# Performance work log

Hardware: AMD Instinct MI355X
Metric: run time of the kernel (lower is better)

Reference implementation:

```python
import jax, jax.numpy as jnp
import numpy as np

H, HD, TOPK = 16, 64, 64

def setup_inputs() -> dict:
    key = jax.random.key(0)
    ks = jax.random.split(key, 6)
    L, B, E = 2048, 2, 1024
    s = 0.02
    return {
        "query": jax.random.normal(ks[0], (L, B, E), jnp.float32),
        "q_w": jax.random.normal(ks[1], (E, E), jnp.float32) * s,
        "q_b": jnp.zeros((E,), jnp.float32),
        "k_w": jax.random.normal(ks[2], (E, E), jnp.float32) * s,
        "k_b": jnp.zeros((E,), jnp.float32),
        "v_w": jax.random.normal(ks[3], (E, E), jnp.float32) * s,
        "v_b": jnp.zeros((E,), jnp.float32),
        "o_w": jax.random.normal(ks[4], (E, E), jnp.float32) * s,
        "o_b": jnp.zeros((E,), jnp.float32),
    }

def reference(query, q_w, q_b, k_w, k_b, v_w, v_b, o_w, o_b):
    L, B, E = query.shape
    scale = HD ** -0.5
    identity = query
    x = jnp.transpose(query, (1, 0, 2))              # [B, L, E]

    def proj(w, b):
        y = x @ w.T + b                              # nn.Linear: x W^T + b
        return jnp.transpose(y.reshape(B, L, H, HD), (0, 2, 1, 3))  # [B,H,L,HD]

    q = proj(q_w, q_b)
    k = proj(k_w, k_b)
    v = proj(v_w, v_b)

    sim_nm = jnp.einsum('bhqd,bhkd->bhqk', q, k) * scale   # full scores [B,H,L,L]
    score_m = sim_nm.sum(axis=2)                           # [B,H,L] per-key score
    _, top_idx = jax.lax.top_k(score_m, TOPK)              # [B,H,TOPK]
    selected_k = jnp.take_along_axis(k, top_idx[..., None], axis=2)  # [B,H,TOPK,HD]

    sim_qn = jax.nn.softmax(jnp.einsum('bhqd,bhmd->bhqm', q, selected_k) * scale, axis=-1)
    sim_km = jax.nn.softmax(jnp.einsum('bhkd,bhmd->bhkm', k, selected_k) * scale, axis=-1)
    sim_qk = jnp.einsum('bhqm,bhkm->bhqk', sim_qn, sim_km)  # [B,H,L,L]
    out = jnp.einsum('bhqk,bhkd->bhqd', sim_qk, v)          # [B,H,L,HD]

    out = jnp.transpose(out, (0, 2, 1, 3)).reshape(B, L, E)
    out = out @ o_w.T + o_b
    out = jnp.transpose(out, (1, 0, 2))                     # back to [L, B, E]
    return identity + out
```

## Files before the change

### kernel.cpp

```cpp
#include <hip/hip_runtime.h>
#include <hip/hip_bf16.h>

#define L_ 2048
#define B_ 2
#define E_ 1024
#define H_ 16
#define HD_ 64
#define TOPK_ 64
#define MROWS (B_*L_)
#define SCALE 0.125f

typedef __attribute__((ext_vector_type(8))) short short8;
typedef __attribute__((ext_vector_type(4))) short short4v;
typedef __attribute__((ext_vector_type(4))) float f32x4;

static __device__ __forceinline__ short f2bf(float f) {
    __hip_bfloat16 h = __float2bfloat16(f);
    return *reinterpret_cast<short*>(&h);
}

__global__ void k_prep(const float* __restrict__ q,
                       const float* __restrict__ w0, const float* __restrict__ w1,
                       const float* __restrict__ w2, const float* __restrict__ w3,
                       short* __restrict__ xb,
                       short* __restrict__ o0, short* __restrict__ o1,
                       short* __restrict__ o2, short* __restrict__ o3,
                       float* __restrict__ xpart) {
    int blk = blockIdx.x;
    if (blk < 512) {
        int cg = blk & 7, ch = blk >> 3;
        int col = cg * 256 + threadIdx.x;
        const float* qp = q + (size_t)(ch * 32) * (B_ * E_) + col;
        float s0 = 0.f, s1 = 0.f, s2 = 0.f, s3 = 0.f;
#pragma unroll
        for (int l = 0; l < 32; l += 4) {
            s0 += qp[(size_t)(l + 0) * (B_ * E_)];
            s1 += qp[(size_t)(l + 1) * (B_ * E_)];
            s2 += qp[(size_t)(l + 2) * (B_ * E_)];
            s3 += qp[(size_t)(l + 3) * (B_ * E_)];
        }
        xpart[ch * (B_ * E_) + col] = (s0 + s1) + (s2 + s3);
    } else if (blk < 4608) {
        int i = (blk - 512) * 256 + threadIdx.x;
        int idx = i * 4;
        int e = idx & (E_ - 1);
        int l = (idx >> 10) & (L_ - 1);
        int b = idx >> 21;
        float4 v = *reinterpret_cast<const float4*>(q + l * (B_ * E_) + b * E_ + e);
        short4v o;
        o[0] = f2bf(v.x); o[1] = f2bf(v.y); o[2] = f2bf(v.z); o[3] = f2bf(v.w);
        *reinterpret_cast<short4v*>(xb + idx) = o;
    } else {
        int cb = blk - 4608;
        int sel = cb >> 10, lb = cb & 1023;
        const float* w = sel == 0 ? w0 : sel == 1 ? w1 : sel == 2 ? w2 : w3;
        short* o = sel == 0 ? o0 : sel == 1 ? o1 : sel == 2 ? o2 : o3;
        int i = lb * 256 + threadIdx.x;
        float4 v = *reinterpret_cast<const float4*>(w + i * 4);
        short4v s;
        s[0] = f2bf(v.x); s[1] = f2bf(v.y); s[2] = f2bf(v.z); s[3] = f2bf(v.w);
        *reinterpret_cast<short4v*>(o + i * 4) = s;
    }
}

template<int MODE, int BM, int BN>
__device__ __forceinline__ void gemm_body(const short* __restrict__ A,
                                          const short* __restrict__ Bw,
                                          const float* __restrict__ bias,
                                          short* __restrict__ Cb,
                                          float* __restrict__ Cf,
                                          const float* __restrict__ ident,
                                          int bx, int by) {
    const int K = E_;
    constexpr int MI = BM / 32;
    constexpr int NI = BN / 64;
    extern __shared__ short smem[];
    short* As = smem;
    short* Bs = smem + 2 * BM * 64;
    int tid = threadIdx.x;
    int lane = tid & 63;
    int wid = tid >> 6;
    int wr = wid >> 2, wc = wid & 3;
    int lrow = lane & 15;
    int kg = lane >> 4;
    int lr8 = lane >> 3;
    int swz = (((lane & 7) ^ (lr8 & 7)) * 8);
    int rx = lrow & 7;
    int mBase = by * BM, nBase = bx * BN;

    auto STAGE = [&](int buf, int k0) {
#pragma unroll
        for (int i = 0; i < BM / 64; ++i) {
            int r0 = (wid * (BM / 64) + i) * 8;
            const short* ga = A + (size_t)(mBase + r0 + lr8) * K + k0 + swz;
            __builtin_amdgcn_global_load_lds(
                (const __attribute__((address_space(1))) void*)ga,
                (__attribute__((address_space(3))) void*)(As + buf * BM * 64 + r0 * 64), 16, 0, 0);
        }
#pragma unroll
        for (int i = 0; i < BN / 64; ++i) {
            int r0 = (wid * (BN / 64) + i) * 8;
            const short* gb = Bw + (size_t)(nBase + r0 + lr8) * K + k0 + swz;
            __builtin_amdgcn_global_load_lds(
                (const __attribute__((address_space(1))) void*)gb,
                (__attribute__((address_space(3))) void*)(Bs + buf * BN * 64 + r0 * 64), 16, 0, 0);
        }
    };

    f32x4 acc[MI][NI];
#pragma unroll
    for (int i = 0; i < MI; ++i)
#pragma unroll
        for (int j = 0; j < NI; ++j) acc[i][j] = (f32x4){0.f, 0.f, 0.f, 0.f};

    STAGE(0, 0);
    asm volatile("s_waitcnt vmcnt(0)" ::: "memory");
    __syncthreads();

    int cur = 0;
    for (int k0 = 0; k0 < K; k0 += 64) {
        if (k0 + 64 < K) STAGE(cur ^ 1, k0 + 64);

        short8 af[2][MI], bf[2][NI];
#pragma unroll
        for (int kk = 0; kk < 2; ++kk) {
#pragma unroll
            for (int mi = 0; mi < MI; ++mi)
                af[kk][mi] = *reinterpret_cast<const short8*>(
                    As + cur * BM * 64 + (wr * (MI * 16) + mi * 16 + lrow) * 64 + (((kk * 4 + kg) ^ rx) * 8));
#pragma unroll
            for (int ni = 0; ni < NI; ++ni)
                bf[kk][ni] = *reinterpret_cast<const short8*>(
                    Bs + cur * BN * 64 + (wc * (NI * 16) + ni * 16 + lrow) * 64 + (((kk * 4 + kg) ^ rx) * 8));
        }
#pragma unroll
        for (int kk = 0; kk < 2; ++kk)
#pragma unroll
            for (int mi = 0; mi < MI; ++mi)
#pragma unroll
                for (int ni = 0; ni < NI; ++ni)
                    acc[mi][ni] = __builtin_amdgcn_mfma_f32_16x16x32_bf16(
                        af[kk][mi], bf[kk][ni], acc[mi][ni], 0, 0, 0);

        asm volatile("s_waitcnt vmcnt(0)" ::: "memory");
        __syncthreads();
        cur ^= 1;
    }

    int rowq = (lane >> 4) * 4;
    int coll = lane & 15;
#pragma unroll
    for (int mi = 0; mi < MI; ++mi) {
#pragma unroll
        for (int ni = 0; ni < NI; ++ni) {
            int col = nBase + wc * (NI * 16) + ni * 16 + coll;
            float bv = bias[col];
            int row0 = mBase + wr * (MI * 16) + mi * 16 + rowq;
            if (MODE == 2) {
                int b = row0 >> 11, l = row0 & (L_ - 1);
                short4v sv;
#pragma unroll
                for (int r = 0; r < 4; ++r) sv[r] = f2bf(acc[mi][ni][r] + bv);
                *reinterpret_cast<short4v*>(
                    Cb + ((size_t)((b * H_ + (col >> 6)) * 64 + (col & 63))) * 2048 + l) = sv;
            } else if (MODE == 1) {
#pragma unroll
                for (int r = 0; r < 4; ++r) {
                    int row = row0 + r;
                    int b = row >> 11, l = row & (L_ - 1);
                    size_t oi = (size_t)l * (B_ * E_) + b * E_ + col;
                    Cf[oi] = acc[mi][ni][r] + bv + ident[oi];
                }
            } else {
#pragma unroll
                for (int r = 0; r < 4; ++r)
                    Cb[(size_t)(row0 + r) * E_ + col] = f2bf(acc[mi][ni][r] + bv);
            }
        }
    }
}

__global__ __launch_bounds__(512) void k_gemm3(const short* __restrict__ A,
    const short* __restrict__ W0, const short* __restrict__ W1, const short* __restrict__ W2,
    const float* __restrict__ b0, const float* __restrict__ b1, const float* __restrict__ b2,
    short* __restrict__ C0, short* __restrict__ C1, short* __restrict__ vtb) {
    int wg = blockIdx.x;
    int sw = (wg & 7) * 96 + (wg >> 3);
    int bx = sw & 7, by = (sw >> 3) & 31, z = sw >> 8;
    if (z == 2)
        gemm_body<2, 128, 128>(A, W2, b2, vtb, nullptr, nullptr, bx, by);
    else if (z == 1)
        gemm_body<0, 128, 128>(A, W1, b1, C1, nullptr, nullptr, bx, by);
    else
        gemm_body<0, 128, 128>(A, W0, b0, C0, nullptr, nullptr, bx, by);
}

__global__ __launch_bounds__(512) void k_gemmo(const short* __restrict__ A,
                                               const short* __restrict__ Bw,
                                               const float* __restrict__ bias,
                                               float* __restrict__ C,
                                               const float* __restrict__ ident) {
    int wg = blockIdx.x;
    int sw = (wg & 7) * 64 + (wg >> 3);
    int bx = sw & 15, by = sw >> 4;
    gemm_body<1, 128, 64>(A, Bw, bias, nullptr, C, ident, bx, by);
}

__global__ __launch_bounds__(256) void k_qt(const float* __restrict__ xpart,
                                            const float* __restrict__ qw,
                                            const float* __restrict__ qb,
                                            const float* __restrict__ kw,
                                            float* __restrict__ tb) {
    __shared__ float xs[1024];
    __shared__ float pr[256];
    __shared__ float qs[64];
    int bh = blockIdx.x;
    int b = bh >> 4, h = bh & 15;
    int tid = threadIdx.x;
    for (int j = tid; j < 1024; j += 256) {
        float s = 0.f;
#pragma unroll
        for (int c = 0; c < 64; ++c) s += xpart[c * (B_ * E_) + b * E_ + j];
        xs[j] = s;
    }
    __syncthreads();
    int fl = tid >> 2, eq = tid & 3;
    int f = h * 64 + fl;
    float s = 0.f;
    for (int e = eq * 256; e < eq * 256 + 256; ++e) s += xs[e] * qw[(size_t)f * E_ + e];
    pr[tid] = s;
    __syncthreads();
    if (eq == 0)
        qs[fl] = ((pr[tid] + pr[tid + 1]) + pr[tid + 2]) + pr[tid + 3] + (float)L_ * qb[f];
    __syncthreads();
    float acc[4] = {0.f, 0.f, 0.f, 0.f};
    for (int d = 0; d < 64; ++d) {
        float qv = qs[d];
        float4 kv = *reinterpret_cast<const float4*>(kw + (size_t)(h * 64 + d) * E_ + tid * 4);
        acc[0] += qv * kv.x; acc[1] += qv * kv.y; acc[2] += qv * kv.z; acc[3] += qv * kv.w;
    }
    float4 o; o.x = acc[0]; o.y = acc[1]; o.z = acc[2]; o.w = acc[3];
    *reinterpret_cast<float4*>(tb + (size_t)bh * E_ + tid * 4) = o;
}

__global__ __launch_bounds__(256) void k_score(const float* __restrict__ query,
                                               const float* __restrict__ tb,
                                               float* __restrict__ scorp) {
    __shared__ float xs[64][68];
    __shared__ float ts[16][68];
    int id = blockIdx.x;
    int eq = id >> 6;
    int b = (id >> 5) & 1;
    int n0 = (id & 31) * 64;
    int tid = threadIdx.x;
    int hg = tid & 3, rg = tid >> 2;
    float acc[4] = {0.f, 0.f, 0.f, 0.f};
    for (int e0 = eq * 256; e0 < eq * 256 + 256; e0 += 64) {
        __syncthreads();
        for (int j = tid; j < 1024; j += 256) {
            int r = j >> 4, c4 = (j & 15) * 4;
            float4 v = *reinterpret_cast<const float4*>(
                &query[(size_t)(n0 + r) * (B_ * E_) + b * E_ + e0 + c4]);
            *reinterpret_cast<float4*>(&xs[r][c4]) = v;
        }
        {
            int hh = tid >> 4, c4 = (tid & 15) * 4;
            float4 v = *reinterpret_cast<const float4*>(&tb[(size_t)(b * 16 + hh) * E_ + e0 + c4]);
            *reinterpret_cast<float4*>(&ts[hh][c4]) = v;
        }
        __syncthreads();
        for (int c = 0; c < 64; ++c) {
            float x0 = xs[rg][c];
#pragma unroll
            for (int j = 0; j < 4; ++j) acc[j] += x0 * ts[hg + 4 * j][c];
        }
    }
#pragma unroll
    for (int j = 0; j < 4; ++j) {
        int h = hg + 4 * j;
        scorp[(size_t)eq * 65536 + (size_t)(b * 16 + h) * L_ + n0 + rg] = acc[j];
    }
}

__global__ __launch_bounds__(256) void k_sel(const float* __restrict__ scorp,
                                             const short* __restrict__ kb,
                                             short* __restrict__ selkb) {
    __shared__ int sel[4][64];
    int tid = threadIdx.x;
    int wid = tid >> 6, lane = tid & 63;
    int bh = blockIdx.x * 4 + wid;
    int b = bh >> 4, h = bh & 15;

    unsigned u[32];
#pragma unroll
    for (int j = 0; j < 32; ++j) {
        int base = bh * L_ + j * 64 + lane;
        float sc = ((scorp[base] + scorp[base + 65536]) + scorp[base + 131072]) + scorp[base + 196608];
        sc *= SCALE;
        unsigned bits = __float_as_uint(sc);
        u[j] = (bits & 0x80000000u) ? ~bits : (bits | 0x80000000u);
    }
    unsigned prefix = 0;
    int k = TOPK_;
    for (int bit = 31; bit >= 0; --bit) {
        unsigned cand = prefix | (1u << bit);
        unsigned cs = cand >> bit;
        int c = 0;
#pragma unroll
        for (int j = 0; j < 32; ++j)
            c += __popcll(__ballot((u[j] >> bit) == cs));
        if (c >= k) prefix = cand; else k -= c;
    }
    unsigned T = prefix;
    int nStrict = 0;
#pragma unroll
    for (int j = 0; j < 32; ++j) nStrict += __popcll(__ballot(u[j] > T));
    int nTies = TOPK_ - nStrict;

    int strictBase = 0, tieBase = 0;
    unsigned long long below = (lane == 0) ? 0ull : ((~0ull) >> (64 - lane));
#pragma unroll
    for (int j = 0; j < 32; ++j) {
        unsigned long long mS = __ballot(u[j] > T);
        unsigned long long mT = __ballot(u[j] == T);
        if (u[j] > T) {
            int slot = strictBase + __popcll(mS & below);
            sel[wid][slot] = j * 64 + lane;
        } else if (u[j] == T) {
            int r = tieBase + __popcll(mT & below);
            if (r < nTies) sel[wid][nStrict + r] = j * 64 + lane;
        }
        strictBase += __popcll(mS);
        tieBase += __popcll(mT);
    }
    __syncthreads();

    int idx8[8];
#pragma unroll
    for (int it = 0; it < 8; ++it) idx8[it] = sel[wid][it * 8 + (lane >> 3)];
#pragma unroll
    for (int it = 0; it < 8; ++it) {
        int m = it * 8 + (lane >> 3);
        const short* src = kb + ((size_t)b * L_ + idx8[it]) * E_ + h * HD_ + (lane & 7) * 8;
        short8 v = *reinterpret_cast<const short8*>(src);
        *reinterpret_cast<short8*>(
            selkb + (size_t)bh * 4096 + m * 64 + (((lane & 7) ^ (m & 7)) * 8)) = v;
    }
}

__global__ __launch_bounds__(256) void k_attW(const short* __restrict__ kb,
                                              const short* __restrict__ vtb,
                                              const short* __restrict__ selkb,
                                              float* __restrict__ wpart) {
    __shared__ short sk[4096], kt[4096], vt[4096], pt[4096];
    int wg = blockIdx.x;
    int sw = (wg & 7) * 64 + (wg >> 3);
    int bh = sw & 31, ch = sw >> 5;
    int b = bh >> 4, h = bh & 15;
    int tid = threadIdx.x, w = tid >> 6, lane = tid & 63;
    int lr = lane & 15, kg = lane >> 4;

#pragma unroll
    for (int j = 0; j < 2; ++j) {
        int off = (w * 2 + j) * 512;
        __builtin_amdgcn_global_load_lds(
            (const __attribute__((address_space(1))) void*)(selkb + (size_t)bh * 4096 + off + lane * 8),
            (__attribute__((address_space(3))) void*)(sk + off), 16, 0, 0);
    }

    f32x4 accw[4];
#pragma unroll
    for (int i = 0; i < 4; ++i) accw[i] = (f32x4){0.f, 0.f, 0.f, 0.f};

    for (int t = 0; t < 2; ++t) {
        int lt = ch * 128 + t * 64;
#pragma unroll
        for (int j = 0; j < 2; ++j) {
            int r = w * 16 + j * 8 + (lane >> 3);
            int s = lane & 7;
            const short* src = kb + ((size_t)(b * L_ + lt + r)) * E_ + h * 64 + ((s ^ (r & 7)) * 8);
            __builtin_amdgcn_global_load_lds(
                (const __attribute__((address_space(1))) void*)src,
                (__attribute__((address_space(3))) void*)(kt + (w * 16 + j * 8) * 64), 16, 0, 0);
        }
        __syncthreads();

        f32x4 s4[4];
#pragma unroll
        for (int i = 0; i < 4; ++i) s4[i] = (f32x4){0.f, 0.f, 0.f, 0.f};
#pragma unroll
        for (int kk = 0; kk < 2; ++kk) {
            int row = w * 16 + lr;
            short8 a = *reinterpret_cast<const short8*>(
                kt + row * 64 + (((kk * 4 + kg) ^ (row & 7)) * 8));
#pragma unroll
            for (int ni = 0; ni < 4; ++ni) {
                int m = ni * 16 + lr;
                short8 bb = *reinterpret_cast<const short8*>(
                    sk + m * 64 + (((kk * 4 + kg) ^ (m & 7)) * 8));
                s4[ni] = __builtin_amdgcn_mfma_f32_16x16x32_bf16(a, bb, s4[ni], 0, 0, 0);
            }
        }
        float p[4][4];
#pragma unroll
        for (int r = 0; r < 4; ++r) {
            float v0 = s4[0][r] * SCALE, v1 = s4[1][r] * SCALE;
            float v2 = s4[2][r] * SCALE, v3 = s4[3][r] * SCALE;
            float mx = fmaxf(fmaxf(v0, v1), fmaxf(v2, v3));
            mx = fmaxf(mx, __shfl_xor(mx, 1));
            mx = fmaxf(mx, __shfl_xor(mx, 2));
            mx = fmaxf(mx, __shfl_xor(mx, 4));
            mx = fmaxf(mx, __shfl_xor(mx, 8));
            float e0 = __expf(v0 - mx), e1 = __expf(v1 - mx);
            float e2 = __expf(v2 - mx), e3 = __expf(v3 - mx);
            float sm = e0 + e1 + e2 + e3;
            sm += __shfl_xor(sm, 1);
            sm += __shfl_xor(sm, 2);
            sm += __shfl_xor(sm, 4);
            sm += __shfl_xor(sm, 8);
            float inv = 1.f / sm;
            p[0][r] = e0 * inv; p[1][r] = e1 * inv; p[2][r] = e2 * inv; p[3][r] = e3 * inv;
        }
#pragma unroll
        for (int ni = 0; ni < 4; ++ni)
#pragma unroll
            for (int r = 0; r < 4; ++r) {
                int m = ni * 16 + lr;
                int ll = w * 16 + kg * 4 + r;
                pt[m * 64 + (((ll >> 3) ^ (m & 7)) * 8) + (ll & 7)] = f2bf(p[ni][r]);
            }
#pragma unroll
        for (int j = 0; j < 2; ++j) {
            int d = w * 16 + j * 8 + (lane >> 3);
            int s = lane & 7;
            const short* src = vtb + ((size_t)(bh * 64 + d)) * 2048 + lt + ((s ^ (d & 7)) * 8);
            __builtin_amdgcn_global_load_lds(
                (const __attribute__((address_space(1))) void*)src,
                (__attribute__((address_space(3))) void*)(vt + (w * 16 + j * 8) * 64), 16, 0, 0);
        }
        __syncthreads();
#pragma unroll
        for (int kk = 0; kk < 2; ++kk) {
            int mm = w * 16 + lr;
            short8 a = *reinterpret_cast<const short8*>(
                pt + mm * 64 + (((kk * 4 + kg) ^ (mm & 7)) * 8));
#pragma unroll
            for (int ni = 0; ni < 4; ++ni) {
                int d = ni * 16 + lr;
                short8 bb = *reinterpret_cast<const short8*>(
                    vt + d * 64 + (((kk * 4 + kg) ^ (d & 7)) * 8));
                accw[ni] = __builtin_amdgcn_mfma_f32_16x16x32_bf16(a, bb, accw[ni], 0, 0, 0);
            }
        }
    }
#pragma unroll
    for (int ni = 0; ni < 4; ++ni)
#pragma unroll
        for (int r = 0; r < 4; ++r) {
            int m = w * 16 + kg * 4 + r;
            int d = ni * 16 + lr;
            wpart[((size_t)(ch * 32 + bh)) * 4096 + m * 64 + d] = accw[ni][r];
        }
}

__global__ void k_wreduce(const float* __restrict__ wpart, short* __restrict__ wtg) {
    int i = blockIdx.x * 256 + threadIdx.x;
    float s = 0.f;
#pragma unroll
    for (int c = 0; c < 16; ++c) s += wpart[(size_t)c * 131072 + i];
    int bh = i >> 12, m = (i >> 6) & 63, d = i & 63;
    wtg[(size_t)bh * 4096 + d * 64 + (((m >> 3) ^ (d & 7)) * 8) + (m & 7)] = f2bf(s);
}

__global__ __launch_bounds__(256) void k_attO(const short* __restrict__ qb,
                                              const short* __restrict__ selkb,
                                              const short* __restrict__ wtg,
                                              short* __restrict__ att) {
    __shared__ short sk[4096], wt[4096], qt[4096], p1[4096];
    int wg = blockIdx.x;
    int sw = (wg & 7) * 64 + (wg >> 3);
    int bh = sw & 31, ch = sw >> 5;
    int b = bh >> 4, h = bh & 15;
    int tid = threadIdx.x, w = tid >> 6, lane = tid & 63;
    int lr = lane & 15, kg = lane >> 4;

#pragma unroll
    for (int j = 0; j < 2; ++j) {
        int off = (w * 2 + j) * 512;
        __builtin_amdgcn_global_load_lds(
            (const __attribute__((address_space(1))) void*)(selkb + (size_t)bh * 4096 + off + lane * 8),
            (__attribute__((address_space(3))) void*)(sk + off), 16, 0, 0);
        __builtin_amdgcn_global_load_lds(
            (const __attribute__((address_space(1))) void*)(wtg + (size_t)bh * 4096 + off + lane * 8),
            (__attribute__((address_space(3))) void*)(wt + off), 16, 0, 0);
    }

    for (int t = 0; t < 2; ++t) {
        int lt = ch * 128 + t * 64;
#pragma unroll
        for (int j = 0; j < 2; ++j) {
            int r = w * 16 + j * 8 + (lane >> 3);
            int s = lane & 7;
            const short* src = qb + ((size_t)(b * L_ + lt + r)) * E_ + h * 64 + ((s ^ (r & 7)) * 8);
            __builtin_amdgcn_global_load_lds(
                (const __attribute__((address_space(1))) void*)src,
                (__attribute__((address_space(3))) void*)(qt + (w * 16 + j * 8) * 64), 16, 0, 0);
        }
        __syncthreads();

        f32x4 s4[4];
#pragma unroll
        for (int i = 0; i < 4; ++i) s4[i] = (f32x4){0.f, 0.f, 0.f, 0.f};
#pragma unroll
        for (int kk = 0; kk < 2; ++kk) {
            int row = w * 16 + lr;
            short8 a = *reinterpret_cast<const short8*>(
                qt + row * 64 + (((kk * 4 + kg) ^ (row & 7)) * 8));
#pragma unroll
            for (int ni = 0; ni < 4; ++ni) {
                int m = ni * 16 + lr;
                short8 bb = *reinterpret_cast<const short8*>(
                    sk + m * 64 + (((kk * 4 + kg) ^ (m & 7)) * 8));
                s4[ni] = __builtin_amdgcn_mfma_f32_16x16x32_bf16(a, bb, s4[ni], 0, 0, 0);
            }
        }
        float p[4][4];
#pragma unroll
        for (int r = 0; r < 4; ++r) {
            float v0 = s4[0][r] * SCALE, v1 = s4[1][r] * SCALE;
            float v2 = s4[2][r] * SCALE, v3 = s4[3][r] * SCALE;
            float mx = fmaxf(fmaxf(v0, v1), fmaxf(v2, v3));
            mx = fmaxf(mx, __shfl_xor(mx, 1));
            mx = fmaxf(mx, __shfl_xor(mx, 2));
            mx = fmaxf(mx, __shfl_xor(mx, 4));
            mx = fmaxf(mx, __shfl_xor(mx, 8));
            float e0 = __expf(v0 - mx), e1 = __expf(v1 - mx);
            float e2 = __expf(v2 - mx), e3 = __expf(v3 - mx);
            float sm = e0 + e1 + e2 + e3;
            sm += __shfl_xor(sm, 1);
            sm += __shfl_xor(sm, 2);
            sm += __shfl_xor(sm, 4);
            sm += __shfl_xor(sm, 8);
            float inv = 1.f / sm;
            p[0][r] = e0 * inv; p[1][r] = e1 * inv; p[2][r] = e2 * inv; p[3][r] = e3 * inv;
        }
#pragma unroll
        for (int ni = 0; ni < 4; ++ni)
#pragma unroll
            for (int r = 0; r < 4; ++r) {
                int m = ni * 16 + lr;
                int ll = w * 16 + kg * 4 + r;
                p1[ll * 64 + (((m >> 3) ^ (ll & 7)) * 8) + (m & 7)] = f2bf(p[ni][r]);
            }
        __syncthreads();
        f32x4 ao[4];
#pragma unroll
        for (int i = 0; i < 4; ++i) ao[i] = (f32x4){0.f, 0.f, 0.f, 0.f};
#pragma unroll
        for (int kk = 0; kk < 2; ++kk) {
            int row = w * 16 + lr;
            short8 a = *reinterpret_cast<const short8*>(
                p1 + row * 64 + (((kk * 4 + kg) ^ (row & 7)) * 8));
#pragma unroll
            for (int ni = 0; ni < 4; ++ni) {
                int d = ni * 16 + lr;
                short8 bb = *reinterpret_cast<const short8*>(
                    wt + d * 64 + (((kk * 4 + kg) ^ (d & 7)) * 8));
                ao[ni] = __builtin_amdgcn_mfma_f32_16x16x32_bf16(a, bb, ao[ni], 0, 0, 0);
            }
        }
#pragma unroll
        for (int ni = 0; ni < 4; ++ni)
#pragma unroll
            for (int r = 0; r < 4; ++r) {
                int l = lt + w * 16 + kg * 4 + r;
                int d = ni * 16 + lr;
                att[((size_t)(b * L_ + l)) * E_ + h * 64 + d] = f2bf(ao[ni][r]);
            }
    }
}

extern "C" void kernel_launch(void* const* d_in, const int* in_sizes, int n_in,
                              void* d_out, int out_size, void* d_ws, size_t ws_size,
                              hipStream_t stream) {
    const float* query = (const float*)d_in[0];
    const float* q_w = (const float*)d_in[1];
    const float* q_b = (const float*)d_in[2];
    const float* k_w = (const float*)d_in[3];
    const float* k_b = (const float*)d_in[4];
    const float* v_w = (const float*)d_in[5];
    const float* v_b = (const float*)d_in[6];
    const float* o_w = (const float*)d_in[7];
    const float* o_b = (const float*)d_in[8];
    float* out = (float*)d_out;

    char* p = (char*)d_ws;
    auto alloc = [&](size_t bytes) {
        char* r = p;
        p += (bytes + 255) & ~(size_t)255;
        return r;
    };
    short* xb    = (short*)alloc((size_t)MROWS * E_ * 2);
    short* qwb   = (short*)alloc((size_t)E_ * E_ * 2);
    short* kwb   = (short*)alloc((size_t)E_ * E_ * 2);
    short* vwb   = (short*)alloc((size_t)E_ * E_ * 2);
    short* owb   = (short*)alloc((size_t)E_ * E_ * 2);
    short* qbuf  = (short*)alloc((size_t)MROWS * E_ * 2);
    short* kbuf  = (short*)alloc((size_t)MROWS * E_ * 2);
    short* vtb   = (short*)alloc((size_t)32 * 64 * 2048 * 2);
    float* xpart = (float*)alloc((size_t)64 * B_ * E_ * 4);
    float* tb    = (float*)alloc((size_t)B_ * H_ * E_ * 4);
    float* scorp = (float*)alloc((size_t)4 * B_ * H_ * L_ * 4);
    short* selkb = (short*)alloc((size_t)32 * 4096 * 2);
    short* wtg   = (short*)alloc((size_t)32 * 4096 * 2);
    float* wpart = (float*)alloc((size_t)16 * 32 * 4096 * 4);
    short* att   = (short*)alloc((size_t)MROWS * E_ * 2);

    k_prep<<<8704, 256, 0, stream>>>(query, q_w, k_w, v_w, o_w, xb, qwb, kwb, vwb, owb, xpart);
    k_qt<<<32, 256, 0, stream>>>(xpart, q_w, q_b, k_w, tb);
    k_score<<<256, 256, 0, stream>>>(query, tb, scorp);

    k_gemm3<<<768, 512, 65536, stream>>>(xb, qwb, kwb, vwb, q_b, k_b, v_b, qbuf, kbuf, vtb);

    k_sel<<<8, 256, 0, stream>>>(scorp, kbuf, selkb);

    k_attW<<<512, 256, 0, stream>>>(kbuf, vtb, selkb, wpart);
    k_wreduce<<<512, 256, 0, stream>>>(wpart, wtg);
    k_attO<<<512, 256, 0, stream>>>(qbuf, selkb, wtg, att);

    k_gemmo<<<512, 512, 49152, stream>>>(att, owb, o_b, out, query);
}
```

Before: 135.9 us.

## Fold score kernel into QKV GEMM launch as extra workgroups

```diff
diff --git a/kernel.cpp b/kernel.cpp
--- a/kernel.cpp
+++ b/kernel.cpp
@@ -180,19 +180,61 @@
     }
 }
 
+__device__ __forceinline__ void score_body(const float* __restrict__ query,
+                                           const float* __restrict__ tb,
+                                           float* __restrict__ scorp, int id) {
+    extern __shared__ short smem[];
+    float* xs = (float*)smem;
+    float* ts = (float*)smem + 64 * 68;
+    int eq = id >> 6;
+    int b = (id >> 5) & 1;
+    int n0 = (id & 31) * 64;
+    int tid = threadIdx.x;
+    int hg = tid & 7, rg = tid >> 3;
+    float acc0 = 0.f, acc1 = 0.f;
+    for (int e0 = eq * 256; e0 < eq * 256 + 256; e0 += 64) {
+        __syncthreads();
+        for (int j = tid; j < 1024; j += 512) {
+            int r = j >> 4, c4 = (j & 15) * 4;
+            float4 v = *reinterpret_cast<const float4*>(
+                &query[(size_t)(n0 + r) * (B_ * E_) + b * E_ + e0 + c4]);
+            *reinterpret_cast<float4*>(&xs[r * 68 + c4]) = v;
+        }
+        if (tid < 256) {
+            int hh = tid >> 4, c4 = (tid & 15) * 4;
+            float4 v = *reinterpret_cast<const float4*>(&tb[(size_t)(b * 16 + hh) * E_ + e0 + c4]);
+            *reinterpret_cast<float4*>(&ts[hh * 68 + c4]) = v;
+        }
+        __syncthreads();
+        for (int c = 0; c < 64; ++c) {
+            float x0 = xs[rg * 68 + c];
+            acc0 += x0 * ts[hg * 68 + c];
+            acc1 += x0 * ts[(hg + 8) * 68 + c];
+        }
+    }
+    scorp[(size_t)eq * 65536 + (size_t)(b * 16 + hg) * L_ + n0 + rg] = acc0;
+    scorp[(size_t)eq * 65536 + (size_t)(b * 16 + hg + 8) * L_ + n0 + rg] = acc1;
+}
+
 __global__ __launch_bounds__(512) void k_gemm3(const short* __restrict__ A,
     const short* __restrict__ W0, const short* __restrict__ W1, const short* __restrict__ W2,
     const float* __restrict__ b0, const float* __restrict__ b1, const float* __restrict__ b2,
-    short* __restrict__ C0, short* __restrict__ C1, short* __restrict__ vtb) {
+    short* __restrict__ C0, short* __restrict__ C1, short* __restrict__ vtb,
+    const float* __restrict__ query, const float* __restrict__ tb,
+    float* __restrict__ scorp) {
     int wg = blockIdx.x;
-    int sw = (wg & 7) * 96 + (wg >> 3);
-    int bx = sw & 7, by = (sw >> 3) & 31, z = sw >> 8;
-    if (z == 2)
-        gemm_body<2, 128, 128>(A, W2, b2, vtb, nullptr, nullptr, bx, by);
-    else if (z == 1)
-        gemm_body<0, 128, 128>(A, W1, b1, C1, nullptr, nullptr, bx, by);
-    else
-        gemm_body<0, 128, 128>(A, W0, b0, C0, nullptr, nullptr, bx, by);
+    if (wg < 768) {
+        int sw = (wg & 7) * 96 + (wg >> 3);
+        int bx = sw & 7, by = (sw >> 3) & 31, z = sw >> 8;
+        if (z == 2)
+            gemm_body<2, 128, 128>(A, W2, b2, vtb, nullptr, nullptr, bx, by);
+        else if (z == 1)
+            gemm_body<0, 128, 128>(A, W1, b1, C1, nullptr, nullptr, bx, by);
+        else
+            gemm_body<0, 128, 128>(A, W0, b0, C0, nullptr, nullptr, bx, by);
+    } else {
+        score_body(query, tb, scorp, wg - 768);
+    }
 }
 
 __global__ __launch_bounds__(512) void k_gemmo(const short* __restrict__ A,
@@ -241,45 +283,6 @@
     }
     float4 o; o.x = acc[0]; o.y = acc[1]; o.z = acc[2]; o.w = acc[3];
     *reinterpret_cast<float4*>(tb + (size_t)bh * E_ + tid * 4) = o;
-}
-
-__global__ __launch_bounds__(256) void k_score(const float* __restrict__ query,
-                                               const float* __restrict__ tb,
-                                               float* __restrict__ scorp) {
-    __shared__ float xs[64][68];
-    __shared__ float ts[16][68];
-    int id = blockIdx.x;
-    int eq = id >> 6;
-    int b = (id >> 5) & 1;
-    int n0 = (id & 31) * 64;
-    int tid = threadIdx.x;
-    int hg = tid & 3, rg = tid >> 2;
-    float acc[4] = {0.f, 0.f, 0.f, 0.f};
-    for (int e0 = eq * 256; e0 < eq * 256 + 256; e0 += 64) {
-        __syncthreads();
-        for (int j = tid; j < 1024; j += 256) {
-            int r = j >> 4, c4 = (j & 15) * 4;
-            float4 v = *reinterpret_cast<const float4*>(
-                &query[(size_t)(n0 + r) * (B_ * E_) + b * E_ + e0 + c4]);
-            *reinterpret_cast<float4*>(&xs[r][c4]) = v;
-        }
-        {
-            int hh = tid >> 4, c4 = (tid & 15) * 4;
-            float4 v = *reinterpret_cast<const float4*>(&tb[(size_t)(b * 16 + hh) * E_ + e0 + c4]);
-            *reinterpret_cast<float4*>(&ts[hh][c4]) = v;
-        }
-        __syncthreads();
-        for (int c = 0; c < 64; ++c) {
-            float x0 = xs[rg][c];
-#pragma unroll
-            for (int j = 0; j < 4; ++j) acc[j] += x0 * ts[hg + 4 * j][c];
-        }
-    }
-#pragma unroll
-    for (int j = 0; j < 4; ++j) {
-        int h = hg + 4 * j;
-        scorp[(size_t)eq * 65536 + (size_t)(b * 16 + h) * L_ + n0 + rg] = acc[j];
-    }
 }
 
 __global__ __launch_bounds__(256) void k_sel(const float* __restrict__ scorp,
@@ -618,9 +621,9 @@
 
     k_prep<<<8704, 256, 0, stream>>>(query, q_w, k_w, v_w, o_w, xb, qwb, kwb, vwb, owb, xpart);
     k_qt<<<32, 256, 0, stream>>>(xpart, q_w, q_b, k_w, tb);
-    k_score<<<256, 256, 0, stream>>>(query, tb, scorp);
-
-    k_gemm3<<<768, 512, 65536, stream>>>(xb, qwb, kwb, vwb, q_b, k_b, v_b, qbuf, kbuf, vtb);
+
+    k_gemm3<<<1024, 512, 65536, stream>>>(xb, qwb, kwb, vwb, q_b, k_b, v_b,
+                                          qbuf, kbuf, vtb, query, tb, scorp);
 
     k_sel<<<8, 256, 0, stream>>>(scorp, kbuf, selkb);
 
```

Result: faster. 126.2 us (median of 3 runs) (-7.2%).
